# Kernel tuning notes

Hardware: AMD Instinct MI355X
Metric: run time of the kernel (lower is better)

The kernel has to match this reference:

```python
import jax, jax.numpy as jnp
import numpy as np

B, C, H, W = 4, 64, 64, 64

def setup_inputs() -> dict:
    key = jax.random.key(0)
    ks = jax.random.split(key, 9)
    return {
        "x": jax.random.normal(ks[0], (B, C, H, W), dtype=jnp.float32),
        "Wq": jax.random.normal(ks[1], (C, C), dtype=jnp.float32) * (1.0 / np.sqrt(C)),
        "bq": jax.random.normal(ks[2], (C,), dtype=jnp.float32) * 0.02,
        "Wk": jax.random.normal(ks[3], (C, C), dtype=jnp.float32) * (1.0 / np.sqrt(C)),
        "bk": jax.random.normal(ks[4], (C,), dtype=jnp.float32) * 0.02,
        "Wv": jax.random.normal(ks[5], (C, C), dtype=jnp.float32) * (1.0 / np.sqrt(C)),
        "bv": jax.random.normal(ks[6], (C,), dtype=jnp.float32) * 0.02,
        "rel_h": jax.random.normal(ks[7], (1, C, H, 1), dtype=jnp.float32),
        "rel_w": jax.random.normal(ks[8], (1, C, 1, W), dtype=jnp.float32),
    }

def reference(x, Wq, bq, Wk, bk, Wv, bv, rel_h, rel_w):
    b, c, h, w = x.shape
    n = h * w
    xf = x.reshape(b, c, n)                                  # [B,C,N]
    # 1x1 convs == channel-wise linear maps (weight [out,in])
    q = jnp.einsum('oc,bcn->bno', Wq, xf) + bq               # [B,N,C]
    k = jnp.einsum('oc,bcn->bon', Wk, xf) + bk[:, None]      # [B,C,N]
    v = jnp.einsum('oc,bcn->bon', Wv, xf) + bv[:, None]      # [B,C,N]
    energy = jnp.einsum('bnc,bcm->bnm', q, k)                # content term [B,N,N]
    pos = (rel_h + rel_w).reshape(c, n)                      # [C,N]
    energy = energy + jnp.einsum('bnc,cm->bnm', q, pos)      # add positional bias
    attn = jax.nn.softmax(energy, axis=-1)                   # [B,N,N]
    # out[b,c,n] = sum_m v[b,c,m] * attn[b,n,m]  (bmm with attention^T)
    out = jnp.einsum('bcm,bnm->bcn', v, attn)
    return out.reshape(b, c, h, w)
```

## Files before the change

kernel.cpp:

```cpp
#include <hip/hip_runtime.h>
#include <math.h>

#define NPOS 4096
#define NB   4
#define NROW (NB * NPOS)
#define SPLIT 4
#define MCHUNK (NPOS / SPLIT)

typedef _Float16 f16;
typedef f16 f16x4 __attribute__((ext_vector_type(4)));
typedef f16 f16x8 __attribute__((ext_vector_type(8)));
typedef float f32x4 __attribute__((ext_vector_type(4)));

#define LDW 72

__global__ __launch_bounds__(256) void qkv_proj(
    const float* __restrict__ x,
    const float* __restrict__ Wq, const float* __restrict__ bq,
    const float* __restrict__ Wk, const float* __restrict__ bk,
    const float* __restrict__ Wv, const float* __restrict__ bv,
    const float* __restrict__ rel_h, const float* __restrict__ rel_w,
    f16* __restrict__ qh, f16* __restrict__ kh, f16* __restrict__ vh)
{
    __shared__ f16 Xs[64 * LDW];
    __shared__ f16 Ws[192 * LDW];

    const int tid = threadIdx.x;
    const int b   = blockIdx.x >> 6;
    const int n0  = (blockIdx.x & 63) << 6;

    #pragma unroll
    for (int k = 0; k < 12; ++k) {
        int idx   = tid + k * 256;
        int orow  = idx >> 4;
        int cseg  = (idx & 15) << 2;
        int mat   = orow >> 6;
        int o     = orow & 63;
        const float* wsrc = (mat == 0) ? Wq : ((mat == 1) ? Wk : Wv);
        float4 v = *(const float4*)(wsrc + o * 64 + cseg);
        f16x4 h; h[0] = (f16)v.x; h[1] = (f16)v.y; h[2] = (f16)v.z; h[3] = (f16)v.w;
        *(f16x4*)(&Ws[orow * LDW + cseg]) = h;
    }
    #pragma unroll
    for (int k = 0; k < 4; ++k) {
        int idx  = tid + k * 256;
        int c    = idx >> 4;
        int nseg = (idx & 15) << 2;
        float4 v = *(const float4*)(x + ((size_t)(b * 64 + c)) * NPOS + n0 + nseg);
        Xs[(nseg + 0) * LDW + c] = (f16)v.x;
        Xs[(nseg + 1) * LDW + c] = (f16)v.y;
        Xs[(nseg + 2) * LDW + c] = (f16)v.z;
        Xs[(nseg + 3) * LDW + c] = (f16)v.w;
    }
    __syncthreads();

    const int wave = tid >> 6;
    const int lane = tid & 63;
    const int quad = lane >> 4;
    const int l16  = lane & 15;

    const f16x8 a0 = *(const f16x8*)(&Xs[(wave * 16 + l16) * LDW + quad * 8]);
    const f16x8 a1 = *(const f16x8*)(&Xs[(wave * 16 + l16) * LDW + 32 + quad * 8]);

    f32x4 acc[12];
    #pragma unroll
    for (int t = 0; t < 12; ++t) {
        f32x4 c0 = {0, 0, 0, 0};
        f16x8 b0 = *(const f16x8*)(&Ws[(t * 16 + l16) * LDW + quad * 8]);
        f16x8 b1 = *(const f16x8*)(&Ws[(t * 16 + l16) * LDW + 32 + quad * 8]);
        c0 = __builtin_amdgcn_mfma_f32_16x16x32_f16(a0, b0, c0, 0, 0, 0);
        c0 = __builtin_amdgcn_mfma_f32_16x16x32_f16(a1, b1, c0, 0, 0, 0);
        acc[t] = c0;
    }

    #pragma unroll
    for (int r = 0; r < 4; ++r) {
        int n = n0 + wave * 16 + quad * 4 + r;
        int h = n >> 6, w = n & 63;
        #pragma unroll
        for (int t = 0; t < 4; ++t) {
            int o = t * 16 + l16;
            qh[((size_t)b * NPOS + n) * 64 + o] = (f16)(acc[t][r] + bq[o]);
        }
        #pragma unroll
        for (int t = 4; t < 8; ++t) {
            int o = (t - 4) * 16 + l16;
            kh[((size_t)b * NPOS + n) * 64 + o] =
                (f16)(acc[t][r] + bk[o] + rel_h[o * 64 + h] + rel_w[o * 64 + w]);
        }
    }

    __syncthreads();
    #pragma unroll
    for (int r = 0; r < 4; ++r) {
        int nl = wave * 16 + quad * 4 + r;
        #pragma unroll
        for (int t = 8; t < 12; ++t) {
            int o = (t - 8) * 16 + l16;
            Xs[o * LDW + nl] = (f16)(acc[t][r] + bv[o]);
        }
    }
    __syncthreads();
    {
        int o  = tid >> 2;
        int ns = (tid & 3) << 4;
        f16* dst = vh + ((size_t)(b * 64 + o)) * NPOS + n0 + ns;
        *(f16x8*)(dst)     = *(const f16x8*)(&Xs[o * LDW + ns]);
        *(f16x8*)(dst + 8) = *(const f16x8*)(&Xs[o * LDW + ns + 8]);
    }
}

#define LDP 72

__global__ __launch_bounds__(256) void attn(
    const f16* __restrict__ qh, const f16* __restrict__ kh,
    const f16* __restrict__ vh,
    f16* __restrict__ Op, float* __restrict__ Mp, float* __restrict__ Lp)
{
    __shared__ f16 Ks[64 * LDP];
    __shared__ f16 Vt[64 * LDP];
    __shared__ f16 Ps[4][16 * LDP];

    const int tid  = threadIdx.x;
    const int wave = tid >> 6;
    const int lane = tid & 63;
    const int quad = lane >> 4;
    const int l16  = lane & 15;
    const int s    = blockIdx.x & (SPLIT - 1);
    const int tile = blockIdx.x / SPLIT;
    const int b    = tile >> 6;
    const int n0   = (tile & 63) << 6;

    const int qrow = n0 + wave * 16 + l16;
    const f16* qbase = qh + ((size_t)b * NPOS + qrow) * 64;
    const f16x8 aq0 = *(const f16x8*)(qbase + quad * 8);
    const f16x8 aq1 = *(const f16x8*)(qbase + 32 + quad * 8);

    f32x4 O[4] = {{0,0,0,0},{0,0,0,0},{0,0,0,0},{0,0,0,0}};
    float m_i[4], l_i[4];
    #pragma unroll
    for (int r = 0; r < 4; ++r) { m_i[r] = -1e30f; l_i[r] = 0.f; }

    const int srow = tid >> 2;
    const int sseg = (tid & 3) * 16;
    const f16* kb = kh + (size_t)b * NPOS * 64;
    const f16* vb = vh + (size_t)b * 64 * NPOS;

    for (int m0 = s * MCHUNK; m0 < (s + 1) * MCHUNK; m0 += 64) {
        const f16* ksrc = kb + (size_t)(m0 + srow) * 64 + sseg;
        *(f16x8*)(&Ks[srow * LDP + sseg])     = *(const f16x8*)(ksrc);
        *(f16x8*)(&Ks[srow * LDP + sseg + 8]) = *(const f16x8*)(ksrc + 8);
        const f16* vsrc = vb + (size_t)srow * NPOS + m0 + sseg;
        *(f16x8*)(&Vt[srow * LDP + sseg])     = *(const f16x8*)(vsrc);
        *(f16x8*)(&Vt[srow * LDP + sseg + 8]) = *(const f16x8*)(vsrc + 8);
        __syncthreads();

        f32x4 S[4];
        #pragma unroll
        for (int t = 0; t < 4; ++t) {
            f32x4 acc = {0, 0, 0, 0};
            f16x8 b0 = *(const f16x8*)(&Ks[(t * 16 + l16) * LDP + quad * 8]);
            f16x8 b1 = *(const f16x8*)(&Ks[(t * 16 + l16) * LDP + 32 + quad * 8]);
            acc = __builtin_amdgcn_mfma_f32_16x16x32_f16(aq0, b0, acc, 0, 0, 0);
            acc = __builtin_amdgcn_mfma_f32_16x16x32_f16(aq1, b1, acc, 0, 0, 0);
            S[t] = acc;
        }

        float p[4][4];
        float alpha[4];
        #pragma unroll
        for (int r = 0; r < 4; ++r) {
            float mx = fmaxf(fmaxf(S[0][r], S[1][r]), fmaxf(S[2][r], S[3][r]));
            #pragma unroll
            for (int d = 1; d <= 8; d <<= 1) mx = fmaxf(mx, __shfl_xor(mx, d));
            float mnew = fmaxf(m_i[r], mx);
            alpha[r] = __expf(m_i[r] - mnew);
            float rs = 0.f;
            #pragma unroll
            for (int t = 0; t < 4; ++t) {
                float e = __expf(S[t][r] - mnew);
                p[t][r] = e;
                rs += e;
            }
            #pragma unroll
            for (int d = 1; d <= 8; d <<= 1) rs += __shfl_xor(rs, d);
            m_i[r] = mnew;
            l_i[r] = l_i[r] * alpha[r] + rs;
        }

        #pragma unroll
        for (int t = 0; t < 4; ++t) {
            #pragma unroll
            for (int r = 0; r < 4; ++r) {
                Ps[wave][(quad * 4 + r) * LDP + t * 16 + l16] = (f16)p[t][r];
                O[t][r] *= alpha[r];
            }
        }

        f16x8 ap0 = *(const f16x8*)(&Ps[wave][l16 * LDP + quad * 8]);
        f16x8 ap1 = *(const f16x8*)(&Ps[wave][l16 * LDP + 32 + quad * 8]);
        #pragma unroll
        for (int t = 0; t < 4; ++t) {
            f16x8 b0 = *(const f16x8*)(&Vt[(t * 16 + l16) * LDP + quad * 8]);
            f16x8 b1 = *(const f16x8*)(&Vt[(t * 16 + l16) * LDP + 32 + quad * 8]);
            O[t] = __builtin_amdgcn_mfma_f32_16x16x32_f16(ap0, b0, O[t], 0, 0, 0);
            O[t] = __builtin_amdgcn_mfma_f32_16x16x32_f16(ap1, b1, O[t], 0, 0, 0);
        }
        __syncthreads();
    }

    #pragma unroll
    for (int r = 0; r < 4; ++r) {
        float inv = 1.f / l_i[r];
        int n = n0 + wave * 16 + quad * 4 + r;
        size_t row = (size_t)b * NPOS + n;
        #pragma unroll
        for (int t = 0; t < 4; ++t) {
            int c = t * 16 + l16;
            Op[((size_t)s * NROW + row) * 64 + c] = (f16)(O[t][r] * inv);
        }
        if (l16 == 0) {
            Mp[(size_t)s * NROW + row] = m_i[r];
            Lp[(size_t)s * NROW + row] = l_i[r];
        }
    }
}

__global__ __launch_bounds__(256) void combine(
    const f16* __restrict__ Op, const float* __restrict__ Mp,
    const float* __restrict__ Lp, float* __restrict__ out)
{
    __shared__ float Ot[64 * 68];

    const int tid = threadIdx.x;
    const int b   = blockIdx.x >> 6;
    const int n0  = (blockIdx.x & 63) << 6;

    {
        int nl = tid >> 2;
        int cs = (tid & 3) << 4;
        size_t row = (size_t)b * NPOS + n0 + nl;

        float m[SPLIT], l[SPLIT];
        float M = -1e30f;
        #pragma unroll
        for (int s = 0; s < SPLIT; ++s) {
            m[s] = Mp[(size_t)s * NROW + row];
            l[s] = Lp[(size_t)s * NROW + row];
            M = fmaxf(M, m[s]);
        }
        float w[SPLIT], L = 0.f;
        #pragma unroll
        for (int s = 0; s < SPLIT; ++s) { w[s] = l[s] * __expf(m[s] - M); L += w[s]; }
        float invL = 1.f / L;

        float val[16];
        #pragma unroll
        for (int j = 0; j < 16; ++j) val[j] = 0.f;
        #pragma unroll
        for (int s = 0; s < SPLIT; ++s) {
            const f16* op = Op + ((size_t)s * NROW + row) * 64 + cs;
            f16x8 o0 = *(const f16x8*)(op);
            f16x8 o1 = *(const f16x8*)(op + 8);
            float ws_ = w[s] * invL;
            #pragma unroll
            for (int j = 0; j < 8; ++j) {
                val[j]     += ws_ * (float)o0[j];
                val[8 + j] += ws_ * (float)o1[j];
            }
        }
        #pragma unroll
        for (int k = 0; k < 4; ++k) {
            float4 v4 = { val[4*k], val[4*k+1], val[4*k+2], val[4*k+3] };
            *(float4*)(&Ot[nl * 68 + cs + 4 * k]) = v4;
        }
    }
    __syncthreads();
    {
        int c  = tid >> 2;
        int ns = (tid & 3) << 4;
        float* dst = out + ((size_t)(b * 64 + c)) * NPOS + n0 + ns;
        #pragma unroll
        for (int k = 0; k < 4; ++k) {
            float4 v4 = { Ot[(ns + 4*k + 0) * 68 + c], Ot[(ns + 4*k + 1) * 68 + c],
                          Ot[(ns + 4*k + 2) * 68 + c], Ot[(ns + 4*k + 3) * 68 + c] };
            *(float4*)(&dst[4 * k]) = v4;
        }
    }
}

extern "C" void kernel_launch(void* const* d_in, const int* in_sizes, int n_in,
                              void* d_out, int out_size, void* d_ws, size_t ws_size,
                              hipStream_t stream) {
    const float* x     = (const float*)d_in[0];
    const float* Wq    = (const float*)d_in[1];
    const float* bq    = (const float*)d_in[2];
    const float* Wk    = (const float*)d_in[3];
    const float* bk    = (const float*)d_in[4];
    const float* Wv    = (const float*)d_in[5];
    const float* bv    = (const float*)d_in[6];
    const float* rel_h = (const float*)d_in[7];
    const float* rel_w = (const float*)d_in[8];
    float* out = (float*)d_out;

    f16* qh = (f16*)d_ws;
    f16* kh = qh + (size_t)NROW * 64;
    f16* vh = kh + (size_t)NROW * 64;
    f16* Op = vh + (size_t)NROW * 64;
    float* Mp = (float*)(Op + (size_t)SPLIT * NROW * 64);
    float* Lp = Mp + (size_t)SPLIT * NROW;

    qkv_proj<<<NB * (NPOS / 64), 256, 0, stream>>>(x, Wq, bq, Wk, bk, Wv, bv,
                                                   rel_h, rel_w, qh, kh, vh);
    attn<<<NB * (NPOS / 64) * SPLIT, 256, 0, stream>>>(qh, kh, vh, Op, Mp, Lp);
    combine<<<NB * (NPOS / 64), 256, 0, stream>>>(Op, Mp, Lp, out);
}
```

Baseline: 143.8 us.

## Transpose score MFMA to keep P in registers, use exp2, raise split to 8

The QK^T product is computed transposed (K as the A operand, Q as B), so each lane holds the scores for one query column. The softmax row max and sum then need only two cross-lane shuffles, and P feeds the PV MFMA (16x16x16) directly from registers, with no LDS round trip. Q is pre-scaled by log2(e) so exp2 replaces expf. The KV split is raised to 8 when the workspace is large enough, and occupancy hints are added. These changes cost extra per-row alpha/l shuffles, twice the partial output traffic in the combine step, and a runtime split loop.

```diff
diff --git a/kernel.cpp b/kernel.cpp
--- a/kernel.cpp
+++ b/kernel.cpp
@@ -4,8 +4,7 @@
 #define NPOS 4096
 #define NB   4
 #define NROW (NB * NPOS)
-#define SPLIT 4
-#define MCHUNK (NPOS / SPLIT)
+#define LOG2E 1.44269504088896f
 
 typedef _Float16 f16;
 typedef f16 f16x4 __attribute__((ext_vector_type(4)));
@@ -31,11 +30,11 @@
 
     #pragma unroll
     for (int k = 0; k < 12; ++k) {
-        int idx   = tid + k * 256;
-        int orow  = idx >> 4;
-        int cseg  = (idx & 15) << 2;
-        int mat   = orow >> 6;
-        int o     = orow & 63;
+        int idx  = tid + k * 256;
+        int orow = idx >> 4;
+        int cseg = (idx & 15) << 2;
+        int mat  = orow >> 6;
+        int o    = orow & 63;
         const float* wsrc = (mat == 0) ? Wq : ((mat == 1) ? Wk : Wv);
         float4 v = *(const float4*)(wsrc + o * 64 + cseg);
         f16x4 h; h[0] = (f16)v.x; h[1] = (f16)v.y; h[2] = (f16)v.z; h[3] = (f16)v.w;
@@ -80,7 +79,7 @@
         #pragma unroll
         for (int t = 0; t < 4; ++t) {
             int o = t * 16 + l16;
-            qh[((size_t)b * NPOS + n) * 64 + o] = (f16)(acc[t][r] + bq[o]);
+            qh[((size_t)b * NPOS + n) * 64 + o] = (f16)((acc[t][r] + bq[o]) * LOG2E);
         }
         #pragma unroll
         for (int t = 4; t < 8; ++t) {
@@ -112,41 +111,39 @@
 
 #define LDP 72
 
-__global__ __launch_bounds__(256) void attn(
+__global__ __launch_bounds__(256, 8) void attn(
     const f16* __restrict__ qh, const f16* __restrict__ kh,
     const f16* __restrict__ vh,
-    f16* __restrict__ Op, float* __restrict__ Mp, float* __restrict__ Lp)
+    f16* __restrict__ Op, float* __restrict__ Mp, float* __restrict__ Lp,
+    int split, int mchunk)
 {
     __shared__ f16 Ks[64 * LDP];
     __shared__ f16 Vt[64 * LDP];
-    __shared__ f16 Ps[4][16 * LDP];
 
     const int tid  = threadIdx.x;
     const int wave = tid >> 6;
     const int lane = tid & 63;
     const int quad = lane >> 4;
     const int l16  = lane & 15;
-    const int s    = blockIdx.x & (SPLIT - 1);
-    const int tile = blockIdx.x / SPLIT;
+    const int s    = blockIdx.x % split;
+    const int tile = blockIdx.x / split;
     const int b    = tile >> 6;
     const int n0   = (tile & 63) << 6;
 
-    const int qrow = n0 + wave * 16 + l16;
-    const f16* qbase = qh + ((size_t)b * NPOS + qrow) * 64;
-    const f16x8 aq0 = *(const f16x8*)(qbase + quad * 8);
-    const f16x8 aq1 = *(const f16x8*)(qbase + 32 + quad * 8);
+    const f16* qbase = qh + ((size_t)b * NPOS + n0 + wave * 16 + l16) * 64;
+    const f16x8 bq0 = *(const f16x8*)(qbase + quad * 8);
+    const f16x8 bq1 = *(const f16x8*)(qbase + 32 + quad * 8);
 
     f32x4 O[4] = {{0,0,0,0},{0,0,0,0},{0,0,0,0},{0,0,0,0}};
-    float m_i[4], l_i[4];
-    #pragma unroll
-    for (int r = 0; r < 4; ++r) { m_i[r] = -1e30f; l_i[r] = 0.f; }
+    float m_i = -1e30f, l_i = 0.f;
 
     const int srow = tid >> 2;
     const int sseg = (tid & 3) * 16;
     const f16* kb = kh + (size_t)b * NPOS * 64;
     const f16* vb = vh + (size_t)b * 64 * NPOS;
 
-    for (int m0 = s * MCHUNK; m0 < (s + 1) * MCHUNK; m0 += 64) {
+    const int m_begin = s * mchunk;
+    for (int m0 = m_begin; m0 < m_begin + mchunk; m0 += 64) {
         const f16* ksrc = kb + (size_t)(m0 + srow) * 64 + sseg;
         *(f16x8*)(&Ks[srow * LDP + sseg])     = *(const f16x8*)(ksrc);
         *(f16x8*)(&Ks[srow * LDP + sseg + 8]) = *(const f16x8*)(ksrc + 8);
@@ -159,76 +156,83 @@
         #pragma unroll
         for (int t = 0; t < 4; ++t) {
             f32x4 acc = {0, 0, 0, 0};
-            f16x8 b0 = *(const f16x8*)(&Ks[(t * 16 + l16) * LDP + quad * 8]);
-            f16x8 b1 = *(const f16x8*)(&Ks[(t * 16 + l16) * LDP + 32 + quad * 8]);
-            acc = __builtin_amdgcn_mfma_f32_16x16x32_f16(aq0, b0, acc, 0, 0, 0);
-            acc = __builtin_amdgcn_mfma_f32_16x16x32_f16(aq1, b1, acc, 0, 0, 0);
+            f16x8 ak0 = *(const f16x8*)(&Ks[(t * 16 + l16) * LDP + quad * 8]);
+            f16x8 ak1 = *(const f16x8*)(&Ks[(t * 16 + l16) * LDP + 32 + quad * 8]);
+            acc = __builtin_amdgcn_mfma_f32_16x16x32_f16(ak0, bq0, acc, 0, 0, 0);
+            acc = __builtin_amdgcn_mfma_f32_16x16x32_f16(ak1, bq1, acc, 0, 0, 0);
             S[t] = acc;
         }
 
+        float mx = S[0][0];
+        #pragma unroll
+        for (int t = 0; t < 4; ++t)
+            #pragma unroll
+            for (int r = 0; r < 4; ++r) mx = fmaxf(mx, S[t][r]);
+        mx = fmaxf(mx, __shfl_xor(mx, 16));
+        mx = fmaxf(mx, __shfl_xor(mx, 32));
+        float mnew  = fmaxf(m_i, mx);
+        float alpha = __builtin_amdgcn_exp2f(m_i - mnew);
         float p[4][4];
-        float alpha[4];
-        #pragma unroll
-        for (int r = 0; r < 4; ++r) {
-            float mx = fmaxf(fmaxf(S[0][r], S[1][r]), fmaxf(S[2][r], S[3][r]));
+        float rs = 0.f;
+        #pragma unroll
+        for (int t = 0; t < 4; ++t)
             #pragma unroll
-            for (int d = 1; d <= 8; d <<= 1) mx = fmaxf(mx, __shfl_xor(mx, d));
-            float mnew = fmaxf(m_i[r], mx);
-            alpha[r] = __expf(m_i[r] - mnew);
-            float rs = 0.f;
-            #pragma unroll
-            for (int t = 0; t < 4; ++t) {
-                float e = __expf(S[t][r] - mnew);
+            for (int r = 0; r < 4; ++r) {
+                float e = __builtin_amdgcn_exp2f(S[t][r] - mnew);
                 p[t][r] = e;
                 rs += e;
             }
+        rs += __shfl_xor(rs, 16);
+        rs += __shfl_xor(rs, 32);
+        m_i = mnew;
+        l_i = l_i * alpha + rs;
+
+        #pragma unroll
+        for (int r = 0; r < 4; ++r) {
+            float av = __shfl(alpha, quad * 20 + r);
+            O[0][r] *= av; O[1][r] *= av; O[2][r] *= av; O[3][r] *= av;
+        }
+
+        f16x4 pa[4];
+        #pragma unroll
+        for (int t = 0; t < 4; ++t) {
+            f16x4 a;
+            a[0] = (f16)p[t][0]; a[1] = (f16)p[t][1];
+            a[2] = (f16)p[t][2]; a[3] = (f16)p[t][3];
+            pa[t] = a;
+        }
+
+        #pragma unroll
+        for (int u = 0; u < 4; ++u) {
             #pragma unroll
-            for (int d = 1; d <= 8; d <<= 1) rs += __shfl_xor(rs, d);
-            m_i[r] = mnew;
-            l_i[r] = l_i[r] * alpha[r] + rs;
-        }
-
-        #pragma unroll
-        for (int t = 0; t < 4; ++t) {
-            #pragma unroll
-            for (int r = 0; r < 4; ++r) {
-                Ps[wave][(quad * 4 + r) * LDP + t * 16 + l16] = (f16)p[t][r];
-                O[t][r] *= alpha[r];
+            for (int t = 0; t < 4; ++t) {
+                f16x4 bf = *(const f16x4*)(&Vt[(u * 16 + l16) * LDP + t * 16 + quad * 4]);
+                O[u] = __builtin_amdgcn_mfma_f32_16x16x16f16(pa[t], bf, O[u], 0, 0, 0);
             }
         }
-
-        f16x8 ap0 = *(const f16x8*)(&Ps[wave][l16 * LDP + quad * 8]);
-        f16x8 ap1 = *(const f16x8*)(&Ps[wave][l16 * LDP + 32 + quad * 8]);
-        #pragma unroll
-        for (int t = 0; t < 4; ++t) {
-            f16x8 b0 = *(const f16x8*)(&Vt[(t * 16 + l16) * LDP + quad * 8]);
-            f16x8 b1 = *(const f16x8*)(&Vt[(t * 16 + l16) * LDP + 32 + quad * 8]);
-            O[t] = __builtin_amdgcn_mfma_f32_16x16x32_f16(ap0, b0, O[t], 0, 0, 0);
-            O[t] = __builtin_amdgcn_mfma_f32_16x16x32_f16(ap1, b1, O[t], 0, 0, 0);
-        }
         __syncthreads();
     }
 
     #pragma unroll
     for (int r = 0; r < 4; ++r) {
-        float inv = 1.f / l_i[r];
+        float lr  = __shfl(l_i, quad * 20 + r);
+        float inv = 1.f / lr;
         int n = n0 + wave * 16 + quad * 4 + r;
         size_t row = (size_t)b * NPOS + n;
         #pragma unroll
-        for (int t = 0; t < 4; ++t) {
-            int c = t * 16 + l16;
-            Op[((size_t)s * NROW + row) * 64 + c] = (f16)(O[t][r] * inv);
-        }
-        if (l16 == 0) {
-            Mp[(size_t)s * NROW + row] = m_i[r];
-            Lp[(size_t)s * NROW + row] = l_i[r];
-        }
+        for (int u = 0; u < 4; ++u)
+            Op[((size_t)s * NROW + row) * 64 + u * 16 + l16] = (f16)(O[u][r] * inv);
+    }
+    if (lane < 16) {
+        size_t row = (size_t)b * NPOS + n0 + wave * 16 + l16;
+        Mp[(size_t)s * NROW + row] = m_i;
+        Lp[(size_t)s * NROW + row] = l_i;
     }
 }
 
 __global__ __launch_bounds__(256) void combine(
     const f16* __restrict__ Op, const float* __restrict__ Mp,
-    const float* __restrict__ Lp, float* __restrict__ out)
+    const float* __restrict__ Lp, float* __restrict__ out, int split)
 {
     __shared__ float Ot[64 * 68];
 
@@ -241,37 +245,32 @@
         int cs = (tid & 3) << 4;
         size_t row = (size_t)b * NPOS + n0 + nl;
 
-        float m[SPLIT], l[SPLIT];
         float M = -1e30f;
-        #pragma unroll
-        for (int s = 0; s < SPLIT; ++s) {
-            m[s] = Mp[(size_t)s * NROW + row];
-            l[s] = Lp[(size_t)s * NROW + row];
-            M = fmaxf(M, m[s]);
-        }
-        float w[SPLIT], L = 0.f;
-        #pragma unroll
-        for (int s = 0; s < SPLIT; ++s) { w[s] = l[s] * __expf(m[s] - M); L += w[s]; }
-        float invL = 1.f / L;
-
+        for (int s2 = 0; s2 < split; ++s2)
+            M = fmaxf(M, Mp[(size_t)s2 * NROW + row]);
+
+        float L = 0.f;
         float val[16];
         #pragma unroll
         for (int j = 0; j < 16; ++j) val[j] = 0.f;
-        #pragma unroll
-        for (int s = 0; s < SPLIT; ++s) {
-            const f16* op = Op + ((size_t)s * NROW + row) * 64 + cs;
+        for (int s2 = 0; s2 < split; ++s2) {
+            float w = Lp[(size_t)s2 * NROW + row] *
+                      __builtin_amdgcn_exp2f(Mp[(size_t)s2 * NROW + row] - M);
+            L += w;
+            const f16* op = Op + ((size_t)s2 * NROW + row) * 64 + cs;
             f16x8 o0 = *(const f16x8*)(op);
             f16x8 o1 = *(const f16x8*)(op + 8);
-            float ws_ = w[s] * invL;
             #pragma unroll
             for (int j = 0; j < 8; ++j) {
-                val[j]     += ws_ * (float)o0[j];
-                val[8 + j] += ws_ * (float)o1[j];
+                val[j]     += w * (float)o0[j];
+                val[8 + j] += w * (float)o1[j];
             }
         }
+        float invL = 1.f / L;
         #pragma unroll
         for (int k = 0; k < 4; ++k) {
-            float4 v4 = { val[4*k], val[4*k+1], val[4*k+2], val[4*k+3] };
+            float4 v4 = { val[4*k] * invL, val[4*k+1] * invL,
+                          val[4*k+2] * invL, val[4*k+3] * invL };
             *(float4*)(&Ot[nl * 68 + cs + 4 * k]) = v4;
         }
     }
@@ -303,15 +302,26 @@
     const float* rel_w = (const float*)d_in[8];
     float* out = (float*)d_out;
 
+    const size_t qkv_elems = (size_t)NROW * 64;
+    int split = 8;
+    {
+        size_t need = 3 * qkv_elems * sizeof(f16)
+                    + (size_t)split * NROW * 64 * sizeof(f16)
+                    + 2 * (size_t)split * NROW * sizeof(float);
+        if (ws_size < need) split = 4;
+    }
+    const int mchunk = NPOS / split;
+
     f16* qh = (f16*)d_ws;
-    f16* kh = qh + (size_t)NROW * 64;
-    f16* vh = kh + (size_t)NROW * 64;
-    f16* Op = vh + (size_t)NROW * 64;
-    float* Mp = (float*)(Op + (size_t)SPLIT * NROW * 64);
-    float* Lp = Mp + (size_t)SPLIT * NROW;
+    f16* kh = qh + qkv_elems;
+    f16* vh = kh + qkv_elems;
+    f16* Op = vh + qkv_elems;
+    float* Mp = (float*)(Op + (size_t)split * NROW * 64);
+    float* Lp = Mp + (size_t)split * NROW;
 
     qkv_proj<<<NB * (NPOS / 64), 256, 0, stream>>>(x, Wq, bq, Wk, bk, Wv, bv,
                                                    rel_h, rel_w, qh, kh, vh);
-    attn<<<NB * (NPOS / 64) * SPLIT, 256, 0, stream>>>(qh, kh, vh, Op, Mp, Lp);
-    combine<<<NB * (NPOS / 64), 256, 0, stream>>>(Op, Mp, Lp, out);
+    attn<<<NB * (NPOS / 64) * split, 256, 0, stream>>>(qh, kh, vh, Op, Mp, Lp,
+                                                       split, mchunk);
+    combine<<<NB * (NPOS / 64), 256, 0, stream>>>(Op, Mp, Lp, out, split);
 }
```

Measured after the change: 128.8 us. 1.12x faster.
